# Kernel optimization log

Measured on AMD Instinct MI355X. Metric: run time of the kernel, lower is better.

## Reference

```python
import jax, jax.numpy as jnp
import numpy as np

NNODES = 6144
DIM = 64
LAYERS = 3
K = 24
ALPHA = 3.0


def setup_inputs() -> dict:
    key = jax.random.key(0)
    ks = jax.random.split(key, 8)
    lin_scale = 1.0 / np.sqrt(DIM)
    return {
        "idx": jnp.arange(NNODES, dtype=jnp.int64) if jax.config.jax_enable_x64 else jnp.arange(NNODES, dtype=jnp.int32),
        "scale_idx": 1,
        "scale_set": jax.random.uniform(ks[0], (LAYERS,), dtype=jnp.float32),
        "emb1": jax.random.normal(ks[1], (NNODES, DIM), dtype=jnp.float32),
        "emb2": jax.random.normal(ks[2], (NNODES, DIM), dtype=jnp.float32),
        "W1": jax.random.uniform(ks[3], (LAYERS, DIM, DIM), dtype=jnp.float32, minval=-lin_scale, maxval=lin_scale),
        "b1": jax.random.uniform(ks[4], (LAYERS, DIM), dtype=jnp.float32, minval=-lin_scale, maxval=lin_scale),
        "W2": jax.random.uniform(ks[5], (LAYERS, DIM, DIM), dtype=jnp.float32, minval=-lin_scale, maxval=lin_scale),
        "b2": jax.random.uniform(ks[6], (LAYERS, DIM), dtype=jnp.float32, minval=-lin_scale, maxval=lin_scale),
    }


def reference(idx, scale_idx, scale_set, emb1, emb2, W1, b1, W2, b2):
    # idx: [N] node ids; scale_idx unused (as in the original forward body)
    n = idx.shape[0]
    nodevec1 = emb1[idx]  # [N, D]
    nodevec2 = emb2[idx]  # [N, D]
    rows = jnp.arange(n)[:, None]  # [N, 1] row indices for scatter
    adj_set = []
    for i in range(LAYERS):
        # per-layer tanh MLP update (state carried across layers)
        nodevec1 = jnp.tanh(ALPHA * ((nodevec1 * scale_set[i]) @ W1[i].T + b1[i]))
        nodevec2 = jnp.tanh(ALPHA * ((nodevec2 * scale_set[i]) @ W2[i].T + b2[i]))
        # antisymmetric similarity: [N, N]
        a = nodevec1 @ nodevec2.T - nodevec2 @ nodevec1.T
        adj0 = jax.nn.relu(jnp.tanh(ALPHA * a))
        # topk per row -> binary mask (scatter of constant 1, matching s1.fill_(1))
        _, t1 = jax.lax.top_k(adj0, K)  # t1: [N, K]
        mask = jnp.zeros((n, n), dtype=adj0.dtype).at[rows, t1].set(1.0)
        adj_set.append(adj0 * mask)
    return jnp.stack(adj_set)  # [LAYERS, N, N]
```

## Files before the change

kernel.cpp:

```cpp
#include <hip/hip_runtime.h>
#include <hip/hip_bf16.h>

#define NN 6144
#define DD 64
#define NL 3
#define KK 24
#define BT2 128
#define KH2 16
#define MB 4
#define KCLAMP 7.99881172180175781f
#define BANDLO 6.5f

typedef unsigned long long ull;

__device__ __forceinline__ float tanh_xla(float x) {
  float xc = fminf(fmaxf(x, -KCLAMP), KCLAMP);
  float x2 = xc * xc;
  float p = -2.76076847742355e-16f;
  p = fmaf(p, x2, 2.00018790482477e-13f);
  p = fmaf(p, x2, -8.60467152213735e-11f);
  p = fmaf(p, x2, 5.12229709037114e-08f);
  p = fmaf(p, x2, 1.48572235717979e-05f);
  p = fmaf(p, x2, 6.37261928875436e-04f);
  p = fmaf(p, x2, 4.89352455891786e-03f);
  p = xc * p;
  float q = 1.19825839466702e-06f;
  q = fmaf(q, x2, 1.18534705686654e-04f);
  q = fmaf(q, x2, 2.26843463243900e-03f);
  q = fmaf(q, x2, 4.89352518554385e-03f);
  float r = p / q;
  return (fabsf(x) < 0.0004f) ? x : r;
}

__device__ __forceinline__ ull shfl_xor_u64(ull v, int m) {
  unsigned lo = __shfl_xor((unsigned)v, m);
  unsigned hi = __shfl_xor((unsigned)(v >> 32), m);
  return ((ull)hi << 32) | lo;
}

__global__ __launch_bounds__(256) void mlp_kernel(
    const int* __restrict__ idx, const float* __restrict__ scale_set,
    const float* __restrict__ emb1, const float* __restrict__ emb2,
    const float* __restrict__ W1, const float* __restrict__ b1,
    const float* __restrict__ W2, const float* __restrict__ b2,
    float* __restrict__ vt1, float* __restrict__ vt2) {
  __shared__ float Wt1[DD][DD];
  __shared__ float Wt2[DD][DD];
  __shared__ float bsh1[DD], bsh2[DD];
  __shared__ __align__(16) float o1sh[MB][DD];
  __shared__ __align__(16) float o2sh[MB][DD];
  const int t = threadIdx.x;
  const int r = t >> 6;
  const int j = t & 63;
  const int grow = blockIdx.x * MB + r;

  {
    int g = idx[grow];
    if (j < 16) {
      ((float4*)&o1sh[r][0])[j] = ((const float4*)(emb1 + (size_t)g * DD))[j];
      ((float4*)&o2sh[r][0])[j] = ((const float4*)(emb2 + (size_t)g * DD))[j];
    }
  }

  for (int l = 0; l < NL; ++l) {
    __syncthreads();
    {
      const float* w1p = W1 + ((size_t)l * DD + j) * DD + r * 16;
      const float* w2p = W2 + ((size_t)l * DD + j) * DD + r * 16;
#pragma unroll
      for (int w = 0; w < 4; ++w) {
        float4 a = *(const float4*)(w1p + 4 * w);
        float4 b = *(const float4*)(w2p + 4 * w);
        int k0 = r * 16 + 4 * w;
        Wt1[k0 + 0][j] = a.x; Wt1[k0 + 1][j] = a.y;
        Wt1[k0 + 2][j] = a.z; Wt1[k0 + 3][j] = a.w;
        Wt2[k0 + 0][j] = b.x; Wt2[k0 + 1][j] = b.y;
        Wt2[k0 + 2][j] = b.z; Wt2[k0 + 3][j] = b.w;
      }
    }
    if (t < DD) { bsh1[t] = b1[l * DD + t]; bsh2[t] = b2[l * DD + t]; }
    __syncthreads();

    const float s = scale_set[l];
    float a1 = 0.0f, a2 = 0.0f;
#pragma unroll
    for (int kb = 0; kb < 16; ++kb) {
      float4 s1 = ((const float4*)&o1sh[r][0])[kb];
      float4 s2 = ((const float4*)&o2sh[r][0])[kb];
      int k0 = 4 * kb;
      a1 = fmaf(s1.x * s, Wt1[k0 + 0][j], a1);
      a1 = fmaf(s1.y * s, Wt1[k0 + 1][j], a1);
      a1 = fmaf(s1.z * s, Wt1[k0 + 2][j], a1);
      a1 = fmaf(s1.w * s, Wt1[k0 + 3][j], a1);
      a2 = fmaf(s2.x * s, Wt2[k0 + 0][j], a2);
      a2 = fmaf(s2.y * s, Wt2[k0 + 1][j], a2);
      a2 = fmaf(s2.z * s, Wt2[k0 + 2][j], a2);
      a2 = fmaf(s2.w * s, Wt2[k0 + 3][j], a2);
    }
    float t1 = tanh_xla(3.0f * (a1 + bsh1[j]));
    float t2 = tanh_xla(3.0f * (a2 + bsh2[j]));
    __syncthreads();
    o1sh[r][j] = t1;
    o2sh[r][j] = t2;
    vt1[((size_t)l * DD + j) * NN + grow] = t1;
    vt2[((size_t)l * DD + j) * NN + grow] = t2;
  }
}

__global__ __launch_bounds__(256) void xmat_kernel(
    const float* __restrict__ vt1, const float* __restrict__ vt2,
    float* __restrict__ out) {
  __shared__ float R1h[KH2][BT2];
  __shared__ float R2h[KH2][BT2];
  __shared__ float C1h[KH2][BT2];
  __shared__ float C2h[KH2][BT2];

  const int a = blockIdx.x;
  const int b = blockIdx.y;
  if (b < a) return;
  const int l = blockIdx.z;
  const int t = threadIdx.x;
  const int r0 = a * BT2;
  const int c0 = b * BT2;
  const float* w1 = vt1 + (size_t)l * DD * NN;
  const float* w2 = vt2 + (size_t)l * DD * NN;
  float* o = out + (size_t)l * NN * NN;

  const int ty = t >> 4;
  const int tx = t & 15;
  const int sk = t >> 4;
  const int sq = (t & 15) * 8;

  float acc1[8][8] = {{0.f}}, acc2[8][8] = {{0.f}};

#pragma unroll
  for (int h = 0; h < 4; ++h) {
    __syncthreads();
    {
      const size_t src = (size_t)(h * KH2 + sk) * NN;
      *(float4*)&R1h[sk][sq]     = *(const float4*)(w1 + src + r0 + sq);
      *(float4*)&R1h[sk][sq + 4] = *(const float4*)(w1 + src + r0 + sq + 4);
      *(float4*)&R2h[sk][sq]     = *(const float4*)(w2 + src + r0 + sq);
      *(float4*)&R2h[sk][sq + 4] = *(const float4*)(w2 + src + r0 + sq + 4);
      *(float4*)&C1h[sk][sq]     = *(const float4*)(w1 + src + c0 + sq);
      *(float4*)&C1h[sk][sq + 4] = *(const float4*)(w1 + src + c0 + sq + 4);
      *(float4*)&C2h[sk][sq]     = *(const float4*)(w2 + src + c0 + sq);
      *(float4*)&C2h[sk][sq + 4] = *(const float4*)(w2 + src + c0 + sq + 4);
    }
    __syncthreads();
#pragma unroll 2
    for (int kk = 0; kk < KH2; ++kk) {
      float r1[8], r2[8], c1[8], c2[8];
      *(float4*)&r1[0] = *(const float4*)&R1h[kk][8 * ty];
      *(float4*)&r1[4] = *(const float4*)&R1h[kk][8 * ty + 4];
      *(float4*)&r2[0] = *(const float4*)&R2h[kk][8 * ty];
      *(float4*)&r2[4] = *(const float4*)&R2h[kk][8 * ty + 4];
      *(float4*)&c1[0] = *(const float4*)&C1h[kk][8 * tx];
      *(float4*)&c1[4] = *(const float4*)&C1h[kk][8 * tx + 4];
      *(float4*)&c2[0] = *(const float4*)&C2h[kk][8 * tx];
      *(float4*)&c2[4] = *(const float4*)&C2h[kk][8 * tx + 4];
#pragma unroll
      for (int i = 0; i < 8; ++i)
#pragma unroll
        for (int j = 0; j < 8; ++j) {
          acc1[i][j] = fmaf(r1[i], c2[j], acc1[i][j]);
          acc2[i][j] = fmaf(r2[i], c1[j], acc2[i][j]);
        }
    }
  }

#pragma unroll
  for (int i = 0; i < 8; ++i) {
    float xv[8];
#pragma unroll
    for (int j = 0; j < 8; ++j) xv[j] = 3.0f * (acc1[i][j] - acc2[i][j]);
    float* p = o + (size_t)(r0 + 8 * ty + i) * NN + c0 + 8 * tx;
    *(float4*)p = *(float4*)&xv[0];
    *(float4*)(p + 4) = *(float4*)&xv[4];
  }
  if (b > a) {
#pragma unroll
    for (int j = 0; j < 8; ++j) {
      float xv[8];
#pragma unroll
      for (int i = 0; i < 8; ++i) xv[i] = 3.0f * (acc2[i][j] - acc1[i][j]);
      float* p = o + (size_t)(c0 + 8 * tx + j) * NN + r0 + 8 * ty;
      *(float4*)p = *(float4*)&xv[0];
      *(float4*)(p + 4) = *(float4*)&xv[4];
    }
  }
}

__global__ __launch_bounds__(256, 2) void topk_kernel(float* __restrict__ out) {
  const int t = threadIdx.x;
  const int w = t >> 6;
  const int lane = t & 63;
  const int row = blockIdx.x * 4 + w;
  float* rp = out + (size_t)row * NN;
  const float Rclamp = tanh_xla(8.0f);
  const unsigned RB = __float_as_uint(Rclamp);
  const ull KOFF = 1ull << 62;
  const ull lmask = (1ull << lane) - 1;

  ull rblo = 0ull, rbhi = 0ull;
  ull sup0 = 0ull, sup1 = 0ull;
  int scnt = 0;

  float4 cur = *(const float4*)(rp + (size_t)lane * 4);
  for (int sb = 0; sb < 24; ++sb) {
    float4 nxt = cur;
    if (sb < 23) nxt = *(const float4*)(rp + (size_t)((sb + 1) * 64 + lane) * 4);
    const float* xp = (const float*)&cur;
    const unsigned gbase = (unsigned)(sb * 256 + lane * 4);

    bool p0 = cur.x >= KCLAMP, p1 = cur.y >= KCLAMP,
         p2 = cur.z >= KCLAMP, p3 = cur.w >= KCLAMP;
    unsigned nib = (p0 ? 1u : 0u) | (p1 ? 2u : 0u) |
                   (p2 ? 4u : 0u) | (p3 ? 8u : 0u);

    bool b0 = (cur.x > BANDLO) & !p0, b1 = (cur.y > BANDLO) & !p1,
         b2 = (cur.z > BANDLO) & !p2, b3 = (cur.w > BANDLO) & !p3;
    if (__any(b0 | b1 | b2 | b3)) {
#pragma unroll
      for (int jj = 0; jj < 4; ++jj) {
        bool bj = (jj == 0) ? b0 : (jj == 1) ? b1 : (jj == 2) ? b2 : b3;
        if (bj) {
          unsigned v = __float_as_uint(tanh_xla(xp[jj]));
          if (v == RB) {
            nib |= 1u << jj;
          } else if (v > RB) {
            ull key = KOFF | ((ull)v << 32) | (ull)(0xFFFFu - (gbase + jj));
            if (scnt == 0) sup0 = key;
            else if (scnt == 1) sup1 = key;
            ++scnt;
          }
        }
      }
    }
    if (sb < 16) rblo |= ((ull)nib) << (sb * 4);
    else         rbhi |= ((ull)nib) << ((sb - 16) * 4);
    cur = nxt;
  }

  ull bs1 = __ballot(scnt >= 1);
  ull bs2 = __ballot(scnt >= 2);
  bool fb = (__ballot(scnt >= 3) != 0ull);
  unsigned S = (unsigned)__popcll(bs1) + (unsigned)__popcll(bs2);
  unsigned E = (S < 24u) ? S : 24u;
  unsigned C24 = 24u - E;

  ull klo = 0ull, khi = 0ull;
  if (!fb && C24 > 0u) {
    unsigned cum = 0;
    for (int sb = 0; sb < 24; ++sb) {
      unsigned nib = (unsigned)((sb < 16 ? (rblo >> (sb * 4))
                                         : (rbhi >> ((sb - 16) * 4))) & 15ull);
      ull bl0 = __ballot((nib & 1u) != 0u);
      ull bl1 = __ballot((nib & 2u) != 0u);
      ull bl2 = __ballot((nib & 4u) != 0u);
      ull bl3 = __ballot((nib & 8u) != 0u);
      unsigned below = (unsigned)__popcll(bl0 & lmask) +
                       (unsigned)__popcll(bl1 & lmask) +
                       (unsigned)__popcll(bl2 & lmask) +
                       (unsigned)__popcll(bl3 & lmask);
      unsigned base = cum + below;
#pragma unroll
      for (int jj = 0; jj < 4; ++jj) {
        if (nib & (1u << jj)) {
          unsigned rk = base + (unsigned)__builtin_popcount(nib & ((1u << jj) - 1u));
          if (rk < C24) {
            if (sb < 16) klo |= 1ull << (sb * 4 + jj);
            else         khi |= 1ull << ((sb - 16) * 4 + jj);
          }
        }
      }
      cum += (unsigned)__popcll(bl0) + (unsigned)__popcll(bl1) +
             (unsigned)__popcll(bl2) + (unsigned)__popcll(bl3);
      if (cum >= C24) break;
    }
    if (cum < C24) fb = true;
  }

  if (!fb) {
    float wv = 0.0f;
    int wi = 0;
    for (unsigned e = 0; e < E; ++e) {
      ull cand = (sup0 > sup1) ? sup0 : sup1;
      ull win = cand;
#pragma unroll
      for (int d = 1; d < 64; d <<= 1) {
        ull o2 = shfl_xor_u64(win, d);
        win = (o2 > win) ? o2 : win;
      }
      if (lane == (int)e) {
        wv = __uint_as_float((unsigned)((win >> 32) & 0x3FFFFFFFu));
        wi = 0xFFFF - (int)(win & 0xFFFFull);
      }
      if (sup0 == win) sup0 = 0ull;
      else if (sup1 == win) sup1 = 0ull;
    }
    float4 z = make_float4(0.f, 0.f, 0.f, 0.f);
    for (int sb = 0; sb < 24; ++sb)
      *(float4*)(rp + (size_t)(sb * 64 + lane) * 4) = z;
    asm volatile("s_waitcnt vmcnt(0)" ::: "memory");
    while (klo) {
      int e = __builtin_ctzll(klo);
      rp[(e >> 2) * 256 + lane * 4 + (e & 3)] = Rclamp;
      klo &= klo - 1;
    }
    while (khi) {
      int e = __builtin_ctzll(khi);
      rp[(16 + (e >> 2)) * 256 + lane * 4 + (e & 3)] = Rclamp;
      khi &= khi - 1;
    }
    if (lane < (int)E && wv > 0.0f) rp[wi] = wv;
    return;
  }

  {
    const ull RKEYHI = (ull)RB << 32;
    const double EMPTYD = __longlong_as_double((long long)KOFF);
    ull mlo = 0ull, mhi = 0ull;
    double s[KK];
#pragma unroll
    for (int q = 0; q < KK; ++q) s[q] = EMPTYD;
    ull s0k = KOFF;

    for (int sb = 0; sb < 24; ++sb) {
      float4 x4 = *(const float4*)(rp + (size_t)(sb * 64 + lane) * 4);
      const float* xp = (const float*)&x4;
      const unsigned gbase = (unsigned)(sb * 256 + lane * 4);
      unsigned nib = 0u;
#pragma unroll
      for (int jj = 0; jj < 4; ++jj) {
        float x = xp[jj];
        if (x >= KCLAMP) {
          nib |= 1u << jj;
        } else if (x > 0.0f) {
          float tv = tanh_xla(x);
          ull key = KOFF | ((ull)__float_as_uint(tv) << 32) |
                    (ull)(0xFFFFu - (gbase + jj));
          if (key > s0k) {
            double kd = __longlong_as_double((long long)key);
#pragma unroll
            for (int i = 0; i < KK - 1; ++i)
              s[i] = fmin(s[i + 1], fmax(s[i], kd));
            s[KK - 1] = fmax(s[KK - 1], kd);
            s0k = (ull)__double_as_longlong(s[0]);
          }
        }
      }
      if (sb < 16) mlo |= ((ull)nib) << (sb * 4);
      else         mhi |= ((ull)nib) << ((sb - 16) * 4);
    }

    float wv = 0.0f;
    int wi = 0;
    for (int r = 0; r < KK; ++r) {
      ull pk = KOFF;
      if (mlo | mhi) {
        int e = mlo ? __builtin_ctzll(mlo) : (64 + __builtin_ctzll(mhi));
        int pidx = ((e >> 2) << 8) + lane * 4 + (e & 3);
        pk = KOFF | RKEYHI | (ull)(0xFFFFu - (unsigned)pidx);
      }
      ull lk = (ull)__double_as_longlong(s[KK - 1]);
      bool fromList = lk > pk;
      ull cand = fromList ? lk : pk;
      ull win = cand;
#pragma unroll
      for (int d = 1; d < 64; d <<= 1) {
        ull o2 = shfl_xor_u64(win, d);
        win = (o2 > win) ? o2 : win;
      }
      if (win == KOFF) break;
      if (lane == r) {
        wv = __uint_as_float((unsigned)((win >> 32) & 0x3FFFFFFFu));
        wi = 0xFFFF - (int)(win & 0xFFFFull);
      }
      if (cand == win) {
        if (fromList) {
#pragma unroll
          for (int i = KK - 1; i > 0; --i) s[i] = s[i - 1];
          s[0] = EMPTYD;
        } else {
          if (mlo) mlo &= mlo - 1;
          else     mhi &= mhi - 1;
        }
      }
    }

    float4 z = make_float4(0.f, 0.f, 0.f, 0.f);
    for (int sb = 0; sb < 24; ++sb)
      *(float4*)(rp + (size_t)(sb * 64 + lane) * 4) = z;
    asm volatile("s_waitcnt vmcnt(0)" ::: "memory");
    if (wv > 0.0f) rp[wi] = wv;
  }
}

extern "C" void kernel_launch(void* const* d_in, const int* in_sizes, int n_in,
                              void* d_out, int out_size, void* d_ws, size_t ws_size,
                              hipStream_t stream) {
  const int*   idx       = (const int*)d_in[0];
  const float* scale_set = (const float*)d_in[2];
  const float* emb1      = (const float*)d_in[3];
  const float* emb2      = (const float*)d_in[4];
  const float* W1        = (const float*)d_in[5];
  const float* b1        = (const float*)d_in[6];
  const float* W2        = (const float*)d_in[7];
  const float* b2        = (const float*)d_in[8];
  float* out = (float*)d_out;

  const size_t VS = (size_t)NL * NN * DD;
  float* vt1 = (float*)d_ws;
  float* vt2 = vt1 + VS;

  mlp_kernel<<<NN / MB, 256, 0, stream>>>(idx, scale_set, emb1, emb2, W1, b1, W2, b2,
                                          vt1, vt2);
  xmat_kernel<<<dim3(NN / BT2, NN / BT2, NL), 256, 0, stream>>>(vt1, vt2, out);
  topk_kernel<<<(NL * NN) / 4, 256, 0, stream>>>(out);
}
```

Baseline: 648.5 us.

## Build per-row clamp bitmaps and super-threshold records in xmat epilogue for topk

The xmat epilogue now classifies each output value while writing it. It packs clamp-saturated hits into per-row bitmaps in workspace and records the few values whose tanh exceeds the clamp value through atomics into per-row slots. The topk kernel then reads these compact bitmaps and records instead of streaming the full 6144-wide row twice. This removes one full read pass of the N×N output per layer. It adds epilogue work, atomics, a larger workspace, and changes the band threshold.

```diff
diff --git a/kernel.cpp b/kernel.cpp
--- a/kernel.cpp
+++ b/kernel.cpp
@@ -9,7 +9,7 @@
 #define KH2 16
 #define MB 4
 #define KCLAMP 7.99881172180175781f
-#define BANDLO 6.5f
+#define BANDLO 7.0f
 
 typedef unsigned long long ull;
 
@@ -43,7 +43,8 @@
     const float* __restrict__ emb1, const float* __restrict__ emb2,
     const float* __restrict__ W1, const float* __restrict__ b1,
     const float* __restrict__ W2, const float* __restrict__ b2,
-    float* __restrict__ vt1, float* __restrict__ vt2) {
+    float* __restrict__ vt1, float* __restrict__ vt2,
+    unsigned* __restrict__ supercnt) {
   __shared__ float Wt1[DD][DD];
   __shared__ float Wt2[DD][DD];
   __shared__ float bsh1[DD], bsh2[DD];
@@ -53,6 +54,8 @@
   const int r = t >> 6;
   const int j = t & 63;
   const int grow = blockIdx.x * MB + r;
+
+  if (t < 12) supercnt[blockIdx.x * 12 + t] = 0u;
 
   {
     int g = idx[grow];
@@ -109,7 +112,8 @@
 
 __global__ __launch_bounds__(256) void xmat_kernel(
     const float* __restrict__ vt1, const float* __restrict__ vt2,
-    float* __restrict__ out) {
+    float* __restrict__ out, ulonglong2* __restrict__ pb,
+    unsigned* __restrict__ supercnt, uint2* __restrict__ superrec) {
   __shared__ float R1h[KH2][BT2];
   __shared__ float R2h[KH2][BT2];
   __shared__ float C1h[KH2][BT2];
@@ -125,6 +129,7 @@
   const float* w1 = vt1 + (size_t)l * DD * NN;
   const float* w2 = vt2 + (size_t)l * DD * NN;
   float* o = out + (size_t)l * NN * NN;
+  const unsigned RB = __float_as_uint(tanh_xla(8.0f));
 
   const int ty = t >> 4;
   const int tx = t & 15;
@@ -169,29 +174,82 @@
     }
   }
 
+  __syncthreads();
+  unsigned char* nibD = (unsigned char*)&C1h[0][0];
+  unsigned char* nibM = ((unsigned char*)&C1h[0][0]) + 2048;
+
 #pragma unroll
   for (int i = 0; i < 8; ++i) {
     float xv[8];
-#pragma unroll
-    for (int j = 0; j < 8; ++j) xv[j] = 3.0f * (acc1[i][j] - acc2[i][j]);
+    unsigned bits = 0;
+#pragma unroll
+    for (int j = 0; j < 8; ++j) {
+      float x = 3.0f * (acc1[i][j] - acc2[i][j]);
+      xv[j] = x;
+      bool rb = (x >= KCLAMP);
+      if (!rb && x > BANDLO) {
+        unsigned vb = __float_as_uint(tanh_xla(x));
+        if (vb == RB) rb = true;
+        else if (vb > RB) {
+          size_t grow = (size_t)l * NN + (r0 + 8 * ty + i);
+          unsigned slot = atomicAdd(&supercnt[grow], 1u);
+          if (slot < 8u)
+            superrec[grow * 8 + slot] = make_uint2(vb, (unsigned)(c0 + 8 * tx + j));
+        }
+      }
+      if (rb) bits |= 1u << j;
+    }
     float* p = o + (size_t)(r0 + 8 * ty + i) * NN + c0 + 8 * tx;
     *(float4*)p = *(float4*)&xv[0];
     *(float4*)(p + 4) = *(float4*)&xv[4];
+    nibD[(8 * ty + i) * 16 + tx] = (unsigned char)bits;
   }
   if (b > a) {
 #pragma unroll
     for (int j = 0; j < 8; ++j) {
       float xv[8];
-#pragma unroll
-      for (int i = 0; i < 8; ++i) xv[i] = 3.0f * (acc2[i][j] - acc1[i][j]);
+      unsigned bits = 0;
+#pragma unroll
+      for (int i = 0; i < 8; ++i) {
+        float x = 3.0f * (acc2[i][j] - acc1[i][j]);
+        xv[i] = x;
+        bool rb = (x >= KCLAMP);
+        if (!rb && x > BANDLO) {
+          unsigned vb = __float_as_uint(tanh_xla(x));
+          if (vb == RB) rb = true;
+          else if (vb > RB) {
+            size_t grow = (size_t)l * NN + (c0 + 8 * tx + j);
+            unsigned slot = atomicAdd(&supercnt[grow], 1u);
+            if (slot < 8u)
+              superrec[grow * 8 + slot] = make_uint2(vb, (unsigned)(r0 + 8 * ty + i));
+          }
+        }
+        if (rb) bits |= 1u << i;
+      }
       float* p = o + (size_t)(c0 + 8 * tx + j) * NN + r0 + 8 * ty;
       *(float4*)p = *(float4*)&xv[0];
       *(float4*)(p + 4) = *(float4*)&xv[4];
-    }
-  }
-}
-
-__global__ __launch_bounds__(256, 2) void topk_kernel(float* __restrict__ out) {
+      nibM[(8 * tx + j) * 16 + ty] = (unsigned char)bits;
+    }
+  }
+  __syncthreads();
+  if (t < 128) {
+    uint4 q = *(const uint4*)&nibD[t * 16];
+    ull lo = (ull)q.x | ((ull)q.y << 32);
+    ull hi = (ull)q.z | ((ull)q.w << 32);
+    pb[((size_t)l * NN + r0 + t) * 48 + b] = make_ulonglong2(lo, hi);
+    if (b > a) {
+      uint4 m = *(const uint4*)&nibM[t * 16];
+      ull mlo = (ull)m.x | ((ull)m.y << 32);
+      ull mhi = (ull)m.z | ((ull)m.w << 32);
+      pb[((size_t)l * NN + c0 + t) * 48 + a] = make_ulonglong2(mlo, mhi);
+    }
+  }
+}
+
+__global__ __launch_bounds__(256, 2) void topk_kernel(
+    const ulonglong2* __restrict__ pb, const unsigned* __restrict__ supercnt,
+    const uint2* __restrict__ superrec, float* __restrict__ out) {
   const int t = threadIdx.x;
   const int w = t >> 6;
   const int lane = t & 63;
@@ -200,93 +258,39 @@
   const float Rclamp = tanh_xla(8.0f);
   const unsigned RB = __float_as_uint(Rclamp);
   const ull KOFF = 1ull << 62;
-  const ull lmask = (1ull << lane) - 1;
-
-  ull rblo = 0ull, rbhi = 0ull;
-  ull sup0 = 0ull, sup1 = 0ull;
-  int scnt = 0;
-
-  float4 cur = *(const float4*)(rp + (size_t)lane * 4);
-  for (int sb = 0; sb < 24; ++sb) {
-    float4 nxt = cur;
-    if (sb < 23) nxt = *(const float4*)(rp + (size_t)((sb + 1) * 64 + lane) * 4);
-    const float* xp = (const float*)&cur;
-    const unsigned gbase = (unsigned)(sb * 256 + lane * 4);
-
-    bool p0 = cur.x >= KCLAMP, p1 = cur.y >= KCLAMP,
-         p2 = cur.z >= KCLAMP, p3 = cur.w >= KCLAMP;
-    unsigned nib = (p0 ? 1u : 0u) | (p1 ? 2u : 0u) |
-                   (p2 ? 4u : 0u) | (p3 ? 8u : 0u);
-
-    bool b0 = (cur.x > BANDLO) & !p0, b1 = (cur.y > BANDLO) & !p1,
-         b2 = (cur.z > BANDLO) & !p2, b3 = (cur.w > BANDLO) & !p3;
-    if (__any(b0 | b1 | b2 | b3)) {
-#pragma unroll
-      for (int jj = 0; jj < 4; ++jj) {
-        bool bj = (jj == 0) ? b0 : (jj == 1) ? b1 : (jj == 2) ? b2 : b3;
-        if (bj) {
-          unsigned v = __float_as_uint(tanh_xla(xp[jj]));
-          if (v == RB) {
-            nib |= 1u << jj;
-          } else if (v > RB) {
-            ull key = KOFF | ((ull)v << 32) | (ull)(0xFFFFu - (gbase + jj));
-            if (scnt == 0) sup0 = key;
-            else if (scnt == 1) sup1 = key;
-            ++scnt;
-          }
-        }
-      }
-    }
-    if (sb < 16) rblo |= ((ull)nib) << (sb * 4);
-    else         rbhi |= ((ull)nib) << ((sb - 16) * 4);
-    cur = nxt;
-  }
-
-  ull bs1 = __ballot(scnt >= 1);
-  ull bs2 = __ballot(scnt >= 2);
-  bool fb = (__ballot(scnt >= 3) != 0ull);
-  unsigned S = (unsigned)__popcll(bs1) + (unsigned)__popcll(bs2);
-  unsigned E = (S < 24u) ? S : 24u;
-  unsigned C24 = 24u - E;
-
-  ull klo = 0ull, khi = 0ull;
-  if (!fb && C24 > 0u) {
-    unsigned cum = 0;
-    for (int sb = 0; sb < 24; ++sb) {
-      unsigned nib = (unsigned)((sb < 16 ? (rblo >> (sb * 4))
-                                         : (rbhi >> ((sb - 16) * 4))) & 15ull);
-      ull bl0 = __ballot((nib & 1u) != 0u);
-      ull bl1 = __ballot((nib & 2u) != 0u);
-      ull bl2 = __ballot((nib & 4u) != 0u);
-      ull bl3 = __ballot((nib & 8u) != 0u);
-      unsigned below = (unsigned)__popcll(bl0 & lmask) +
-                       (unsigned)__popcll(bl1 & lmask) +
-                       (unsigned)__popcll(bl2 & lmask) +
-                       (unsigned)__popcll(bl3 & lmask);
-      unsigned base = cum + below;
-#pragma unroll
-      for (int jj = 0; jj < 4; ++jj) {
-        if (nib & (1u << jj)) {
-          unsigned rk = base + (unsigned)__builtin_popcount(nib & ((1u << jj) - 1u));
-          if (rk < C24) {
-            if (sb < 16) klo |= 1ull << (sb * 4 + jj);
-            else         khi |= 1ull << ((sb - 16) * 4 + jj);
-          }
-        }
-      }
-      cum += (unsigned)__popcll(bl0) + (unsigned)__popcll(bl1) +
-             (unsigned)__popcll(bl2) + (unsigned)__popcll(bl3);
-      if (cum >= C24) break;
-    }
-    if (cum < C24) fb = true;
-  }
+
+  ull bmx = 0ull, bmy = 0ull;
+  if (lane < 48) {
+    ulonglong2 bmv = pb[(size_t)row * 48 + lane];
+    bmx = bmv.x; bmy = bmv.y;
+  }
+  const unsigned S = supercnt[row];
+  bool fb = (S > 8u);
+  const unsigned E = (S < 24u) ? S : 24u;
+  const unsigned C24 = 24u - E;
+
+  ull skey = 0ull;
+  if (!fb && lane < (int)S) {
+    uint2 rec = superrec[(size_t)row * 8 + lane];
+    skey = KOFF | ((ull)rec.x << 32) | (ull)(0xFFFFu - rec.y);
+  }
+
+  unsigned cnt = (unsigned)__popcll(bmx) + (unsigned)__popcll(bmy);
+  unsigned p = cnt;
+#pragma unroll
+  for (int d = 1; d < 64; d <<= 1) {
+    unsigned o2 = __shfl_up(p, d);
+    if (lane >= d) p += o2;
+  }
+  unsigned excl = p - cnt;
+  unsigned total = __shfl(p, 63);
+  if (total < C24) fb = true;
 
   if (!fb) {
     float wv = 0.0f;
     int wi = 0;
     for (unsigned e = 0; e < E; ++e) {
-      ull cand = (sup0 > sup1) ? sup0 : sup1;
-      ull win = cand;
+      ull win = skey;
 #pragma unroll
       for (int d = 1; d < 64; d <<= 1) {
         ull o2 = shfl_xor_u64(win, d);
@@ -296,22 +300,29 @@
         wv = __uint_as_float((unsigned)((win >> 32) & 0x3FFFFFFFu));
         wi = 0xFFFF - (int)(win & 0xFFFFull);
       }
-      if (sup0 == win) sup0 = 0ull;
-      else if (sup1 == win) sup1 = 0ull;
+      if (skey == win) skey = 0ull;
     }
     float4 z = make_float4(0.f, 0.f, 0.f, 0.f);
     for (int sb = 0; sb < 24; ++sb)
       *(float4*)(rp + (size_t)(sb * 64 + lane) * 4) = z;
     asm volatile("s_waitcnt vmcnt(0)" ::: "memory");
-    while (klo) {
-      int e = __builtin_ctzll(klo);
-      rp[(e >> 2) * 256 + lane * 4 + (e & 3)] = Rclamp;
-      klo &= klo - 1;
-    }
-    while (khi) {
-      int e = __builtin_ctzll(khi);
-      rp[(16 + (e >> 2)) * 256 + lane * 4 + (e & 3)] = Rclamp;
-      khi &= khi - 1;
+    int need = (int)C24 - (int)excl;
+    if (need > (int)cnt) need = (int)cnt;
+    if (need > 0 && lane < 48) {
+      int base = lane * 128;
+      int done = 0;
+      ull m = bmx;
+      while (done < need && m) {
+        int k = __builtin_ctzll(m);
+        rp[base + k] = Rclamp;
+        m &= m - 1; ++done;
+      }
+      m = bmy;
+      while (done < need && m) {
+        int k = __builtin_ctzll(m);
+        rp[base + 64 + k] = Rclamp;
+        m &= m - 1; ++done;
+      }
     }
     if (lane < (int)E && wv > 0.0f) rp[wi] = wv;
     return;
@@ -413,9 +424,13 @@
   const size_t VS = (size_t)NL * NN * DD;
   float* vt1 = (float*)d_ws;
   float* vt2 = vt1 + VS;
+  ulonglong2* pb = (ulonglong2*)(vt2 + VS);
+  unsigned* supercnt = (unsigned*)(pb + (size_t)NL * NN * 48);
+  uint2* superrec = (uint2*)(supercnt + (size_t)NL * NN);
 
   mlp_kernel<<<NN / MB, 256, 0, stream>>>(idx, scale_set, emb1, emb2, W1, b1, W2, b2,
-                                          vt1, vt2);
-  xmat_kernel<<<dim3(NN / BT2, NN / BT2, NL), 256, 0, stream>>>(vt1, vt2, out);
-  topk_kernel<<<(NL * NN) / 4, 256, 0, stream>>>(out);
-}
+                                          vt1, vt2, supercnt);
+  xmat_kernel<<<dim3(NN / BT2, NN / BT2, NL), 256, 0, stream>>>(
+      vt1, vt2, out, pb, supercnt, superrec);
+  topk_kernel<<<(NL * NN) / 4, 256, 0, stream>>>(pb, supercnt, superrec, out);
+}
```

After: 630.5 us. -2.8%, faster.
